# Kernel optimization log

Hardware: AMD Instinct MI355X
Metric: run time of the kernel (lower is better)

The kernel has to match this reference:

```python
import jax, jax.numpy as jnp
import numpy as np

B, N, E_PER = 2048, 64, 512            # graphs, nodes/graph, edges/graph
D_NODE, D_EMB = 16, 64                 # env.node_state_dim, node_embedding_size
D_USER, D_UEMB = 32, 64                # env.user_state_dim, user_embedding_size
HID = 512
TOTAL_N, TOTAL_E = B * N, B * E_PER


def setup_inputs() -> dict:
    key = jax.random.key(0)
    ks = jax.random.split(key, 16)
    off = (jnp.arange(B, dtype=jnp.int32) * N)[:, None]
    src = jax.random.randint(ks[0], (B, E_PER), 0, N, dtype=jnp.int32) + off
    dst = jax.random.randint(ks[1], (B, E_PER), 0, N, dtype=jnp.int32) + off
    edge_index = jnp.stack([src.reshape(-1), dst.reshape(-1)])  # [2, TOTAL_E]
    s = lambda k, shape, sc=0.05: jax.random.normal(k, shape, jnp.float32) * sc
    return {
        "x": jax.random.normal(ks[2], (TOTAL_N, D_NODE), jnp.float32),
        "edge_attr": jax.random.normal(ks[3], (TOTAL_E, 2), jnp.float32),
        "user_s": jax.random.normal(ks[4], (B, D_USER), jnp.float32),
        "W_msg": s(ks[5], (D_NODE, D_EMB)), "b_msg": jnp.zeros((D_EMB,), jnp.float32),
        "W_edge": s(ks[6], (2, D_EMB)),     "b_edge": jnp.zeros((D_EMB,), jnp.float32),
        "W_self": s(ks[7], (D_NODE, D_EMB)),"b_self": jnp.zeros((D_EMB,), jnp.float32),
        "W1": s(ks[8], (D_USER, D_UEMB)),   "b1": jnp.zeros((D_UEMB,), jnp.float32),
        "W2": s(ks[9], (N * D_EMB + D_UEMB, HID)), "b2": jnp.zeros((HID,), jnp.float32),
        "W3": s(ks[10], (HID, HID // 2)),   "b3": jnp.zeros((HID // 2,), jnp.float32),
        "W4": s(ks[11], (HID // 2, N), 0.01), "b4": jnp.zeros((N,), jnp.float32),
        "edge_index": edge_index,
    }


def reference(x, edge_attr, user_s, W_msg, b_msg, W_edge, b_edge, W_self, b_self,
              W1, b1, W2, b2, W3, b3, W4, b4, edge_index):
    src, dst = edge_index[0], edge_index[1]
    # GeneralConv (PyG): msg = lin_msg(x_j) + lin_edge(e); sum-aggregate at dst; + lin_self(x_i)
    msg = x[src] @ W_msg + b_msg + edge_attr @ W_edge + b_edge          # [TOTAL_E, D_EMB]
    agg = jax.ops.segment_sum(msg, dst, num_segments=TOTAL_N)          # [TOTAL_N, D_EMB]
    node = jax.nn.relu(agg + x @ W_self + b_self)
    # F.dropout(p=0.5, training=True) -- deterministic mask for the reference
    keep = jax.random.bernoulli(jax.random.key(42), 0.5, node.shape)
    node = jnp.where(keep, node * 2.0, 0.0)
    user = jax.nn.relu(user_s @ W1 + b1)                               # [B, D_UEMB]
    states = jnp.concatenate([node.reshape(B, N * D_EMB), user], axis=1)
    h = jax.nn.relu(states @ W2 + b2)
    h = jax.nn.relu(h @ W3 + b3)
    logits = h @ W4 + b4                                               # [B, N]
    # torch: unsqueeze(dim=0) then softmax(dim=1) => softmax across the BATCH axis
    return jax.nn.softmax(logits, axis=0)[None]                        # [1, B, N]
```

## Files before the change

kernel.cpp:

```cpp
#include <hip/hip_runtime.h>
#include <stdint.h>

#define B_GRAPHS 2048
#define CHUNK 256
#define E_PER 512
#define D_USER 32
#define HID 512
#define GK 4160
#define STATES_DIM 4160
#define WS_FALLBACK 6356992
#define WS_FAST 56197120

typedef unsigned short u16;
typedef unsigned int u32;
typedef __attribute__((ext_vector_type(8))) short short8;
typedef __attribute__((ext_vector_type(4))) float f32x4;

__device__ __forceinline__ float bf2f(u16 b) {
    union { uint32_t u; float f; } c; c.u = ((uint32_t)b) << 16; return c.f;
}
__device__ __forceinline__ u16 f2bf(float f) {
    union { float f; uint32_t u; } c; c.f = f;
    uint32_t u = c.u;
    return (u16)((u + 0x7FFFu + ((u >> 16) & 1u)) >> 16);
}
__device__ __forceinline__ void unpack2(uint32_t w, float& lo, float& hi) {
    union { uint32_t u; float f; } a, b;
    a.u = w << 16; b.u = w & 0xFFFF0000u;
    lo = a.f; hi = b.f;
}

__device__ __forceinline__ uint32_t rotl32(uint32_t v, int r) {
    return (v << r) | (v >> (32 - r));
}
__device__ __forceinline__ void threefry_0_42(uint32_t x0, uint32_t x1,
                                              uint32_t& o0, uint32_t& o1) {
    const uint32_t ks0 = 0u, ks1 = 42u, ks2 = 0x1BD11BDAu ^ 42u;
    x0 += ks0; x1 += ks1;
#define TFR(r) { x0 += x1; x1 = rotl32(x1, (r)); x1 ^= x0; }
    TFR(13) TFR(15) TFR(26) TFR(6)
    x0 += ks1; x1 += ks2 + 1u;
    TFR(17) TFR(29) TFR(16) TFR(24)
    x0 += ks2; x1 += ks0 + 2u;
    TFR(13) TFR(15) TFR(26) TFR(6)
    x0 += ks0; x1 += ks1 + 3u;
    TFR(17) TFR(29) TFR(16) TFR(24)
    x0 += ks1; x1 += ks2 + 4u;
    TFR(13) TFR(15) TFR(26) TFR(6)
    x0 += ks2; x1 += ks0 + 5u;
#undef TFR
    o0 = x0; o1 = x1;
}
__device__ __forceinline__ bool keep_bit(uint32_t j) {
    uint32_t o0, o1;
    threefry_0_42(0u, j, o0, o1);
    return (((o0 ^ o1) >> 31) == 0u);
}

__global__ __launch_bounds__(256) void fill_kernel(float* __restrict__ out, float v, int n) {
    int i = blockIdx.x * 256 + threadIdx.x;
    if (i < n) out[i] = v;
}

__device__ __forceinline__ void trans32(float (*sT)[33],
                                        const float* __restrict__ W,
                                        u16* __restrict__ WT,
                                        int K, int N, int k0, int n0, int tid) {
    const int tr = tid >> 5, tc = tid & 31;
    #pragma unroll
    for (int i = 0; i < 32; i += 8)
        sT[tr + i][tc] = W[(size_t)(k0 + tr + i) * N + n0 + tc];
    __syncthreads();
    #pragma unroll
    for (int i = 0; i < 32; i += 8)
        WT[(size_t)(n0 + tr + i) * K + k0 + tc] = f2bf(sT[tc][tr + i]);
}

#define SM_SCNT  0
#define SM_SXT   8192
#define SM_SA2   10496
#define SM_WCAT  15616
#define SM_ESUM  20736
#define SM_DEG   21248
#define SM_SIZE  21504

__global__ __launch_bounds__(256) void node_prep(
    const float* __restrict__ x, const float* __restrict__ edge_attr,
    const float* __restrict__ user_s,
    const float* __restrict__ W_msg, const float* __restrict__ W_self,
    const float* __restrict__ b_msg, const float* __restrict__ W_edge,
    const float* __restrict__ b_edge, const float* __restrict__ b_self,
    const float* __restrict__ W1, const float* __restrict__ b1,
    const int* __restrict__ src, const int* __restrict__ dst,
    const float* __restrict__ W2, u16* __restrict__ W2T,
    const float* __restrict__ W3, u16* __restrict__ W3T,
    const float* __restrict__ W4, u16* __restrict__ W4T,
    u16* __restrict__ states)
{
    __shared__ __align__(16) char smem[SM_SIZE];
    const int tid = threadIdx.x;

    if (blockIdx.x >= B_GRAPHS) {
        float (*sT)[33] = (float(*)[33])smem;
        int b = blockIdx.x - B_GRAPHS;
        if (b < 2080) {
            trans32(sT, W2, W2T, 4160, 512, (b % 130) * 32, (b / 130) * 32, tid);
            return;
        }
        b -= 2080;
        if (b < 128) {
            trans32(sT, W3, W3T, 512, 256, (b % 16) * 32, (b / 16) * 32, tid);
            return;
        }
        b -= 128;
        trans32(sT, W4, W4T, 256, 64, (b % 8) * 32, (b / 8) * 32, tid);
        return;
    }

    u32 (*scnt)[32]  = (u32(*)[32])(smem + SM_SCNT);
    u16 (*sxT)[72]   = (u16(*)[72])(smem + SM_SXT);
    u16 (*sA2)[40]   = (u16(*)[40])(smem + SM_SA2);
    u16* sWcat       = (u16*)(smem + SM_WCAT);
    float (*sesum)[64] = (float(*)[64])(smem + SM_ESUM);
    float* sdeg      = (float*)(smem + SM_DEG);

    const int g = blockIdx.x;
    const int w = tid >> 6, lane = tid & 63;
    const int lm = lane & 15, q = lane >> 4;

    const float* xg = x + (size_t)g * 1024;
    const float4 xv = *(const float4*)&xg[tid * 4];
    const int ge0 = g * E_PER + tid, ge1 = ge0 + 256;
    const int s0 = src[ge0] - g * 64, d0 = dst[ge0] - g * 64;
    const int s1 = src[ge1] - g * 64, d1 = dst[ge1] - g * 64;
    const float2* ea2 = (const float2*)edge_attr;
    const float2 a0 = ea2[ge0], a1 = ea2[ge1];
    float bs[4], bm[4], we0[4], we1[4];
    #pragma unroll
    for (int nt = 0; nt < 4; ++nt) {
        int e = nt * 16 + lm;
        bs[nt]  = b_self[e];
        bm[nt]  = b_msg[e] + b_edge[e];
        we0[nt] = W_edge[e];
        we1[nt] = W_edge[64 + e];
    }
    {
        uint4 z = make_uint4(0, 0, 0, 0);
        u32* c0 = &scnt[0][0] + tid * 8;
        *(uint4*)(c0) = z; *(uint4*)(c0 + 4) = z;
    }
    if (tid < 128) ((float*)sesum)[tid] = 0.f;
    {
        #pragma unroll
        for (int i = 0; i < 8; ++i) {
            int idx = tid + 256 * i;
            int e = idx >> 5, k = idx & 31;
            float v = (k < 16) ? W_msg[k * 64 + e] : W_self[(k - 16) * 64 + e];
            sWcat[e * 40 + k] = f2bf(v);
        }
    }
    {
        const int n = tid >> 2, kb = (tid & 3) * 4;
        u16 x0 = f2bf(xv.x), x1 = f2bf(xv.y), x2 = f2bf(xv.z), x3 = f2bf(xv.w);
        sxT[kb + 0][n] = x0; sxT[kb + 1][n] = x1;
        sxT[kb + 2][n] = x2; sxT[kb + 3][n] = x3;
        *(ushort4*)&sA2[n][16 + kb] = make_ushort4(x0, x1, x2, x3);
    }
    __syncthreads();

    atomicAdd(&scnt[d0][(s0 >> 1) ^ ((d0 & 7) << 2)], 1u << ((s0 & 1) * 16));
    atomicAdd(&scnt[d1][(s1 >> 1) ^ ((d1 & 7) << 2)], 1u << ((s1 & 1) * 16));
    atomicAdd(&sesum[0][d0], a0.x);
    atomicAdd(&sesum[1][d0], a0.y);
    atomicAdd(&sesum[0][d1], a1.x);
    atomicAdd(&sesum[1][d1], a1.y);
    __syncthreads();

    {
        const int d = tid >> 2, sq = tid & 3;
        uint4 c0 = *(const uint4*)&scnt[d][sq * 8];
        uint4 c1 = *(const uint4*)&scnt[d][sq * 8 + 4];
        u32 cw[8] = {c0.x, c0.y, c0.z, c0.w, c1.x, c1.y, c1.z, c1.w};
        u32 pk[8];
        float degp = 0.f;
        #pragma unroll
        for (int j = 0; j < 8; ++j) {
            u32 lo = cw[j] & 0xFFFFu, hi = cw[j] >> 16;
            degp += (float)(lo + hi);
            pk[j] = (u32)f2bf((float)lo) | ((u32)f2bf((float)hi) << 16);
        }
        *(uint4*)&scnt[d][sq * 8]     = make_uint4(pk[0], pk[1], pk[2], pk[3]);
        *(uint4*)&scnt[d][sq * 8 + 4] = make_uint4(pk[4], pk[5], pk[6], pk[7]);
        degp += __shfl_xor(degp, 1, 64);
        degp += __shfl_xor(degp, 2, 64);
        if (sq == 0) sdeg[d] = degp;
    }

    f32x4 accS;
    #pragma unroll
    for (int r = 0; r < 4; ++r) accS[r] = 0.f;
    {
        const char* crow = (const char*)&scnt[16 * w + lm][0];
        const int sw = (lm & 7) << 4;
        #pragma unroll
        for (int kh = 0; kh < 2; ++kh) {
            short8 a = *(const short8*)(crow + (((kh * 64) + q * 16) ^ sw));
            short8 b = *(const short8*)&sxT[lm][kh * 32 + q * 8];
            accS = __builtin_amdgcn_mfma_f32_16x16x32_bf16(a, b, accS, 0, 0, 0);
        }
    }
    #pragma unroll
    for (int r = 0; r < 4; ++r)
        sA2[16 * w + q * 4 + r][lm] = f2bf(accS[r]);

    f32x4 acc2[4];
    #pragma unroll
    for (int nt = 0; nt < 4; ++nt)
        #pragma unroll
        for (int r = 0; r < 4; ++r) acc2[nt][r] = 0.f;
    short8 a2 = *(const short8*)&sA2[16 * w + lm][q * 8];
    #pragma unroll
    for (int nt = 0; nt < 4; ++nt) {
        short8 b2 = *(const short8*)&sWcat[(nt * 16 + lm) * 40 + q * 8];
        acc2[nt] = __builtin_amdgcn_mfma_f32_16x16x32_bf16(a2, b2, acc2[nt], 0, 0, 0);
    }

    u16* out = states + (size_t)g * STATES_DIM;
    #pragma unroll
    for (int r = 0; r < 4; ++r) {
        int n = 16 * w + q * 4 + r;
        float dg = sdeg[n], e0 = sesum[0][n], e1 = sesum[1][n];
        uint32_t jbase = (uint32_t)g * 4096u + (uint32_t)(n * 64 + lm);
        #pragma unroll
        for (int nt = 0; nt < 4; ++nt) {
            float v = acc2[nt][r] + bs[nt] + dg * bm[nt]
                    + e0 * we0[nt] + e1 * we1[nt];
            v = v > 0.f ? v : 0.f;
            v = keep_bit(jbase + (uint32_t)(nt * 16)) ? v * 2.0f : 0.0f;
            out[n * 64 + nt * 16 + lm] = f2bf(v);
        }
    }
    if (tid < 64) {
        float v = b1[tid];
        const float* us = user_s + (size_t)g * D_USER;
        #pragma unroll
        for (int k = 0; k < D_USER; ++k) v += us[k] * W1[k * 64 + tid];
        out[4096 + tid] = f2bf(v > 0.f ? v : 0.f);
    }
}

__global__ __launch_bounds__(256) void node_fb(
    int g0,
    const float* __restrict__ x, const float* __restrict__ edge_attr,
    const float* __restrict__ user_s,
    const float* __restrict__ W_msg, const float* __restrict__ b_msg,
    const float* __restrict__ W_edge, const float* __restrict__ b_edge,
    const float* __restrict__ W_self, const float* __restrict__ b_self,
    const float* __restrict__ W1, const float* __restrict__ b1,
    const int* __restrict__ src, const int* __restrict__ dst,
    float* __restrict__ states)
{
    const int g = g0 + blockIdx.x;
    const int tid = threadIdx.x;

    __shared__ float sx[64][16];
    __shared__ float sxsum[64][16];
    __shared__ float sesum[64][2];
    __shared__ float sdeg[64];
    __shared__ float sWmsg[16][64];
    __shared__ float sWself[16][64];
    __shared__ float sWedge[2][64];
    __shared__ float sbias[64];
    __shared__ float sbself[64];

    const float* xg = x + (size_t)g * 1024;
    for (int i = tid; i < 1024; i += 256) {
        sx[i >> 4][i & 15] = xg[i];
        ((float*)sxsum)[i] = 0.f;
        ((float*)sWmsg)[i] = W_msg[i];
        ((float*)sWself)[i] = W_self[i];
    }
    if (tid < 128) ((float*)sWedge)[tid] = W_edge[tid];
    if (tid < 64) {
        sbias[tid] = b_msg[tid] + b_edge[tid];
        sbself[tid] = b_self[tid];
        sdeg[tid] = 0.f;
        sesum[tid][0] = 0.f; sesum[tid][1] = 0.f;
    }
    __syncthreads();

    const float2* ea2 = (const float2*)edge_attr;
    for (int e = tid; e < E_PER; e += 256) {
        int ge = g * E_PER + e;
        int s = src[ge] - g * 64;
        int d = dst[ge] - g * 64;
        float2 a = ea2[ge];
        atomicAdd(&sdeg[d], 1.0f);
        atomicAdd(&sesum[d][0], a.x);
        atomicAdd(&sesum[d][1], a.y);
        #pragma unroll
        for (int k = 0; k < 16; ++k) atomicAdd(&sxsum[d][k], sx[s][k]);
    }
    __syncthreads();

    float* out = states + (size_t)blockIdx.x * STATES_DIM;
    #pragma unroll
    for (int i = 0; i < 16; ++i) {
        int idx = tid + 256 * i;
        int n = idx >> 6, e = idx & 63;
        float v = sbself[e] + sdeg[n] * sbias[e]
                + sesum[n][0] * sWedge[0][e] + sesum[n][1] * sWedge[1][e];
        #pragma unroll
        for (int k = 0; k < 16; ++k)
            v += sxsum[n][k] * sWmsg[k][e] + sx[n][k] * sWself[k][e];
        v = v > 0.f ? v : 0.f;
        v = keep_bit((uint32_t)g * 4096u + (uint32_t)idx) ? v * 2.0f : 0.0f;
        out[idx] = v;
    }
    if (tid < 64) {
        float v = b1[tid];
        const float* us = user_s + (size_t)g * D_USER;
        #pragma unroll
        for (int k = 0; k < D_USER; ++k) v += us[k] * W1[k * 64 + tid];
        out[4096 + tid] = v > 0.f ? v : 0.f;
    }
}

__global__ __launch_bounds__(256) void gemm64(
    const u16* __restrict__ A, const u16* __restrict__ BT,
    float* __restrict__ Cpart, int K, int Ksplit, int N, int ntiles,
    int pstride)
{
    const int cpx = gridDim.x >> 3;
    const int bid = blockIdx.x;
    const int wg  = (bid & 7) * cpx + (bid >> 3);
    const int nt  = wg % ntiles, mt = wg / ntiles;
    const int m0 = mt * 64, n0 = nt * 64;
    const int kb = blockIdx.y * Ksplit;

    __shared__ u16 sA[64][72];
    __shared__ u16 sB[64][72];

    const int tid = threadIdx.x;
    const int wave = tid >> 6, lane = tid & 63;
    const int wm = (wave & 1) * 32, wn = (wave >> 1) * 32;
    const int lm = lane & 15, q = lane >> 4;

    f32x4 acc00, acc01, acc10, acc11;
    #pragma unroll
    for (int r = 0; r < 4; ++r) {
        acc00[r] = 0.f; acc01[r] = 0.f; acc10[r] = 0.f; acc11[r] = 0.f;
    }

    const int arow = tid >> 2, aseg = (tid & 3) * 16;
    const u16* pa = &A [(size_t)(m0 + arow) * K + kb + aseg];
    const u16* pb = &BT[(size_t)(n0 + arow) * K + kb + aseg];
    uint4 ra0 = *(const uint4*)pa, ra1 = *(const uint4*)(pa + 8);
    uint4 rb0 = *(const uint4*)pb, rb1 = *(const uint4*)(pb + 8);

    for (int k0 = 0; k0 < Ksplit; k0 += 64) {
        __syncthreads();
        *(uint4*)&sA[arow][aseg]     = ra0;
        *(uint4*)&sA[arow][aseg + 8] = ra1;
        *(uint4*)&sB[arow][aseg]     = rb0;
        *(uint4*)&sB[arow][aseg + 8] = rb1;
        __syncthreads();
        if (k0 + 64 < Ksplit) {
            pa += 64; pb += 64;
            ra0 = *(const uint4*)pa; ra1 = *(const uint4*)(pa + 8);
            rb0 = *(const uint4*)pb; rb1 = *(const uint4*)(pb + 8);
        }
        #pragma unroll
        for (int kh = 0; kh < 2; ++kh) {
            short8 a0 = *(const short8*)&sA[wm + lm]     [kh * 32 + q * 8];
            short8 a1 = *(const short8*)&sA[wm + 16 + lm][kh * 32 + q * 8];
            short8 b0 = *(const short8*)&sB[wn + lm]     [kh * 32 + q * 8];
            short8 b1 = *(const short8*)&sB[wn + 16 + lm][kh * 32 + q * 8];
            acc00 = __builtin_amdgcn_mfma_f32_16x16x32_bf16(a0, b0, acc00, 0, 0, 0);
            acc01 = __builtin_amdgcn_mfma_f32_16x16x32_bf16(a0, b1, acc01, 0, 0, 0);
            acc10 = __builtin_amdgcn_mfma_f32_16x16x32_bf16(a1, b0, acc10, 0, 0, 0);
            acc11 = __builtin_amdgcn_mfma_f32_16x16x32_bf16(a1, b1, acc11, 0, 0, 0);
        }
    }

    float* Cp = Cpart + (size_t)blockIdx.y * pstride;
    #pragma unroll
    for (int r = 0; r < 4; ++r) {
        int m = m0 + wm + q * 4 + r;
        Cp[(size_t)m * N + n0 + wn + lm]              = acc00[r];
        Cp[(size_t)m * N + n0 + wn + 16 + lm]         = acc01[r];
        Cp[(size_t)(m + 16) * N + n0 + wn + lm]       = acc10[r];
        Cp[(size_t)(m + 16) * N + n0 + wn + 16 + lm]  = acc11[r];
    }
}

__global__ __launch_bounds__(256) void bias_relu_sum(
    const float* __restrict__ parts, int pstride, int nsplit,
    const float* __restrict__ bias, u16* __restrict__ out,
    int Nmask, int total4)
{
    int i = blockIdx.x * 256 + threadIdx.x;
    if (i >= total4) return;
    const int base = i * 4;
    float4 v = *(const float4*)&bias[base & Nmask];
    for (int s = 0; s < nsplit; ++s) {
        float4 p = *(const float4*)&parts[(size_t)s * pstride + base];
        v.x += p.x; v.y += p.y; v.z += p.z; v.w += p.w;
    }
    ushort4 o;
    o.x = f2bf(v.x > 0.f ? v.x : 0.f);
    o.y = f2bf(v.y > 0.f ? v.y : 0.f);
    o.z = f2bf(v.z > 0.f ? v.z : 0.f);
    o.w = f2bf(v.w > 0.f ? v.w : 0.f);
    *(ushort4*)&out[base] = o;
}

template<typename AT, typename CT, bool RELU>
__global__ __launch_bounds__(256) void gemm_any(
    const AT* __restrict__ A, const float* __restrict__ B,
    const float* __restrict__ bias, CT* __restrict__ C,
    int M, int N, int K)
{
    __shared__ float sA[32][72];
    __shared__ float sB[32][64];

    const int tid = threadIdx.x;
    const int tx = tid & 15;
    const int ty = tid >> 4;
    const int m0 = blockIdx.x * 64, n0 = blockIdx.y * 64;

    float acc[4][4] = {};

    for (int k0 = 0; k0 < K; k0 += 32) {
        if constexpr (sizeof(AT) == 4) {
            int r = tid >> 3;
            int c = (tid & 7) * 4;
            #pragma unroll
            for (int rr = 0; rr < 64; rr += 32) {
                float4 v = *(const float4*)&((const float*)A)[(size_t)(m0 + r + rr) * K + k0 + c];
                sA[c + 0][r + rr] = v.x; sA[c + 1][r + rr] = v.y;
                sA[c + 2][r + rr] = v.z; sA[c + 3][r + rr] = v.w;
            }
        } else {
            int m = tid >> 2;
            int c = (tid & 3) * 8;
            uint4 v = *(const uint4*)&((const u16*)A)[(size_t)(m0 + m) * K + k0 + c];
            unpack2(v.x, sA[c + 0][m], sA[c + 1][m]);
            unpack2(v.y, sA[c + 2][m], sA[c + 3][m]);
            unpack2(v.z, sA[c + 4][m], sA[c + 5][m]);
            unpack2(v.w, sA[c + 6][m], sA[c + 7][m]);
        }
        {
            int r = tid >> 3;
            int nc = (tid & 7) * 8;
            float4 v0 = *(const float4*)&B[(size_t)(k0 + r) * N + n0 + nc];
            float4 v1 = *(const float4*)&B[(size_t)(k0 + r) * N + n0 + nc + 4];
            sB[r][nc + 0] = v0.x; sB[r][nc + 1] = v0.y;
            sB[r][nc + 2] = v0.z; sB[r][nc + 3] = v0.w;
            sB[r][nc + 4] = v1.x; sB[r][nc + 5] = v1.y;
            sB[r][nc + 6] = v1.z; sB[r][nc + 7] = v1.w;
        }
        __syncthreads();
        #pragma unroll
        for (int kk = 0; kk < 32; ++kk) {
            float4 av = *(const float4*)&sA[kk][ty * 4];
            float4 bv = *(const float4*)&sB[kk][tx * 4];
            float a_[4] = {av.x, av.y, av.z, av.w};
            float b_[4] = {bv.x, bv.y, bv.z, bv.w};
            #pragma unroll
            for (int i = 0; i < 4; ++i)
                #pragma unroll
                for (int j = 0; j < 4; ++j)
                    acc[i][j] += a_[i] * b_[j];
        }
        __syncthreads();
    }

    #pragma unroll
    for (int i = 0; i < 4; ++i) {
        int m = m0 + ty * 4 + i;
        #pragma unroll
        for (int j = 0; j < 4; ++j) {
            int n = n0 + tx * 4 + j;
            float v = acc[i][j] + bias[n];
            if (RELU) v = v > 0.f ? v : 0.f;
            if constexpr (sizeof(CT) == 2) C[(size_t)m * N + n] = (CT)f2bf(v);
            else                           C[(size_t)m * N + n] = (CT)v;
        }
    }
}

__global__ __launch_bounds__(256) void softmax4(
    const float* __restrict__ parts, const float* __restrict__ b4,
    float* __restrict__ out)
{
    const int n = blockIdx.x;
    const int tid = threadIdx.x;
    __shared__ float sred[4];
    const int wid = tid >> 6, lane = tid & 63;
    const float bn = b4[n];

    float v[8];
    #pragma unroll
    for (int i = 0; i < 8; ++i) {
        int row = (tid + 256 * i) * 64 + n;
        float t = bn + parts[row] + parts[131072 + row]
                + parts[262144 + row] + parts[393216 + row];
        v[i] = (t > -1e30f && t < 1e30f) ? t : 0.0f;
    }

    float mx = -3.4e38f;
    #pragma unroll
    for (int i = 0; i < 8; ++i) mx = fmaxf(mx, v[i]);
    #pragma unroll
    for (int off = 32; off > 0; off >>= 1) mx = fmaxf(mx, __shfl_down(mx, off, 64));
    if (lane == 0) sred[wid] = mx;
    __syncthreads();
    if (tid == 0) sred[0] = fmaxf(fmaxf(sred[0], sred[1]), fmaxf(sred[2], sred[3]));
    __syncthreads();
    mx = sred[0];
    __syncthreads();

    float sum = 0.f;
    #pragma unroll
    for (int i = 0; i < 8; ++i) { v[i] = expf(v[i] - mx); sum += v[i]; }
    #pragma unroll
    for (int off = 32; off > 0; off >>= 1) sum += __shfl_down(sum, off, 64);
    if (lane == 0) sred[wid] = sum;
    __syncthreads();
    if (tid == 0) sred[0] = sred[0] + sred[1] + sred[2] + sred[3];
    __syncthreads();
    float inv = 1.0f / sred[0];
    #pragma unroll
    for (int i = 0; i < 8; ++i) out[(tid + 256 * i) * 64 + n] = v[i] * inv;
}

__global__ __launch_bounds__(256) void softmax_kernel(
    const float* __restrict__ logits, float* __restrict__ out)
{
    const int n = blockIdx.x;
    const int tid = threadIdx.x;
    __shared__ float sred[4];
    const int wid = tid >> 6, lane = tid & 63;

    float v[8];
    #pragma unroll
    for (int i = 0; i < 8; ++i) {
        float t = logits[(tid + 256 * i) * 64 + n];
        v[i] = (t > -1e30f && t < 1e30f) ? t : 0.0f;
    }

    float mx = -3.4e38f;
    #pragma unroll
    for (int i = 0; i < 8; ++i) mx = fmaxf(mx, v[i]);
    #pragma unroll
    for (int off = 32; off > 0; off >>= 1) mx = fmaxf(mx, __shfl_down(mx, off, 64));
    if (lane == 0) sred[wid] = mx;
    __syncthreads();
    if (tid == 0) sred[0] = fmaxf(fmaxf(sred[0], sred[1]), fmaxf(sred[2], sred[3]));
    __syncthreads();
    mx = sred[0];
    __syncthreads();

    float sum = 0.f;
    #pragma unroll
    for (int i = 0; i < 8; ++i) { v[i] = expf(v[i] - mx); sum += v[i]; }
    #pragma unroll
    for (int off = 32; off > 0; off >>= 1) sum += __shfl_down(sum, off, 64);
    if (lane == 0) sred[wid] = sum;
    __syncthreads();
    if (tid == 0) sred[0] = sred[0] + sred[1] + sred[2] + sred[3];
    __syncthreads();
    float inv = 1.0f / sred[0];
    #pragma unroll
    for (int i = 0; i < 8; ++i) out[(tid + 256 * i) * 64 + n] = v[i] * inv;
}

extern "C" void kernel_launch(void* const* d_in, const int* in_sizes, int n_in,
                              void* d_out, int out_size, void* d_ws, size_t ws_size,
                              hipStream_t stream) {
    if (ws_size < (size_t)WS_FALLBACK || n_in < 18) {
        fill_kernel<<<(out_size + 255) / 256, 256, 0, stream>>>((float*)d_out, 0.25f, out_size);
        return;
    }
    {
        const int expect[18] = {2097152, 2097152, 65536, 1024, 64, 128, 64,
                                1024, 64, 2048, 64, 2129920, 512, 131072, 256,
                                16384, 64, 2097152};
        bool ok = true;
        for (int i = 0; i < 18; ++i) ok = ok && (in_sizes[i] == expect[i]);
        if (!ok || out_size != 131072) {
            fill_kernel<<<(out_size + 255) / 256, 256, 0, stream>>>((float*)d_out, 0.125f, out_size);
            return;
        }
    }

    const float* x         = (const float*)d_in[0];
    const float* edge_attr = (const float*)d_in[1];
    const float* user_s    = (const float*)d_in[2];
    const float* W_msg     = (const float*)d_in[3];
    const float* b_msg     = (const float*)d_in[4];
    const float* W_edge    = (const float*)d_in[5];
    const float* b_edge    = (const float*)d_in[6];
    const float* W_self    = (const float*)d_in[7];
    const float* b_self    = (const float*)d_in[8];
    const float* W1        = (const float*)d_in[9];
    const float* b1        = (const float*)d_in[10];
    const float* W2        = (const float*)d_in[11];
    const float* b2        = (const float*)d_in[12];
    const float* W3        = (const float*)d_in[13];
    const float* b3        = (const float*)d_in[14];
    const float* W4        = (const float*)d_in[15];
    const float* b4        = (const float*)d_in[16];
    const int* edge_index  = (const int*)d_in[17];
    const int* src = edge_index;
    const int* dst = edge_index + B_GRAPHS * E_PER;

    float* logits = (float*)d_out;
    char* ws = (char*)d_ws;

    if (ws_size >= (size_t)WS_FAST) {
        u16*   states = (u16*)ws;
        u16*   W2T    = (u16*)(ws + 17039360);
        float* h2part = (float*)(ws + 21299200);
        u16*   h2     = (u16*)(ws + 42270720);
        u16*   W3T    = (u16*)(ws + 44367872);
        float* h3part = (float*)(ws + 44630016);
        u16*   h3     = (u16*)(ws + 53018624);
        u16*   W4T    = (u16*)(ws + 54067200);
        float* lpart  = (float*)(ws + 54099968);

        node_prep<<<B_GRAPHS + 2224, 256, 0, stream>>>(
            x, edge_attr, user_s, W_msg, W_self, b_msg, W_edge, b_edge,
            b_self, W1, b1, src, dst, W2, W2T, W3, W3T, W4, W4T, states);
        gemm64<<<dim3(256, 5), 256, 0, stream>>>(states, W2T, h2part,
                                                 GK, 832, 512, 8, 1048576);
        bias_relu_sum<<<1024, 256, 0, stream>>>(h2part, 1048576, 5, b2, h2,
                                                511, 262144);
        gemm64<<<dim3(128, 4), 256, 0, stream>>>(h2, W3T, h3part,
                                                 512, 128, 256, 4, 524288);
        bias_relu_sum<<<512, 256, 0, stream>>>(h3part, 524288, 4, b3, h3,
                                               255, 131072);
        gemm64<<<dim3(32, 4), 256, 0, stream>>>(h3, W4T, lpart,
                                                256, 64, 64, 1, 131072);
        softmax4<<<64, 256, 0, stream>>>(lpart, b4, logits);
    } else {
        float* states = (float*)ws;
        float* h3     = (float*)ws;
        u16*   h2     = (u16*)(ws + 4259840);

        for (int c = 0; c < B_GRAPHS / CHUNK; ++c) {
            node_fb<<<CHUNK, 256, 0, stream>>>(
                c * CHUNK, x, edge_attr, user_s, W_msg, b_msg, W_edge, b_edge,
                W_self, b_self, W1, b1, src, dst, states);
            gemm_any<float, u16, true><<<dim3(CHUNK / 64, HID / 64), 256, 0, stream>>>(
                states, W2, b2, h2 + (size_t)c * CHUNK * HID, CHUNK, HID, STATES_DIM);
        }
        gemm_any<u16,   float, true ><<<dim3(32, 4), 256, 0, stream>>>(
            h2, W3, b3, h3, B_GRAPHS, HID / 2, HID);
        gemm_any<float, float, false><<<dim3(32, 1), 256, 0, stream>>>(
            h3, W4, b4, logits, B_GRAPHS, 64, HID / 2);
        softmax_kernel<<<64, 256, 0, stream>>>(logits, logits);
    }
}
```

Measured before the change: 174.7 us.

## Use direct global-to-LDS loads with swizzle in GEMM, fuse final layer into softmax

Result: slower. 192.1 us (+9.9%).

```diff
diff --git a/kernel.cpp b/kernel.cpp
--- a/kernel.cpp
+++ b/kernel.cpp
@@ -9,7 +9,7 @@
 #define GK 4160
 #define STATES_DIM 4160
 #define WS_FALLBACK 6356992
-#define WS_FAST 56197120
+#define WS_FAST 54067200
 
 typedef unsigned short u16;
 typedef unsigned int u32;
@@ -28,6 +28,12 @@
     union { uint32_t u; float f; } a, b;
     a.u = w << 16; b.u = w & 0xFFFF0000u;
     lo = a.f; hi = b.f;
+}
+
+__device__ __forceinline__ void gload16(const u16* g, u16* l) {
+    __builtin_amdgcn_global_load_lds(
+        (const __attribute__((address_space(1))) void*)g,
+        (__attribute__((address_space(3))) void*)l, 16, 0, 0);
 }
 
 __device__ __forceinline__ uint32_t rotl32(uint32_t v, int r) {
@@ -94,7 +100,6 @@
     const int* __restrict__ src, const int* __restrict__ dst,
     const float* __restrict__ W2, u16* __restrict__ W2T,
     const float* __restrict__ W3, u16* __restrict__ W3T,
-    const float* __restrict__ W4, u16* __restrict__ W4T,
     u16* __restrict__ states)
 {
     __shared__ __align__(16) char smem[SM_SIZE];
@@ -105,15 +110,10 @@
         int b = blockIdx.x - B_GRAPHS;
         if (b < 2080) {
             trans32(sT, W2, W2T, 4160, 512, (b % 130) * 32, (b / 130) * 32, tid);
-            return;
-        }
-        b -= 2080;
-        if (b < 128) {
+        } else {
+            b -= 2080;
             trans32(sT, W3, W3T, 512, 256, (b % 16) * 32, (b / 16) * 32, tid);
-            return;
-        }
-        b -= 128;
-        trans32(sT, W4, W4T, 256, 64, (b % 8) * 32, (b / 8) * 32, tid);
+        }
         return;
     }
 
@@ -150,6 +150,15 @@
         *(uint4*)(c0) = z; *(uint4*)(c0 + 4) = z;
     }
     if (tid < 128) ((float*)sesum)[tid] = 0.f;
+    u32 kmask = 0;
+    #pragma unroll
+    for (int r = 0; r < 4; ++r) {
+        const uint32_t jb = (uint32_t)g * 4096u
+                          + (uint32_t)((16 * w + q * 4 + r) * 64 + lm);
+        #pragma unroll
+        for (int nt = 0; nt < 4; ++nt)
+            if (keep_bit(jb + (uint32_t)(nt * 16))) kmask |= 1u << (r * 4 + nt);
+    }
     {
         #pragma unroll
         for (int i = 0; i < 8; ++i) {
@@ -230,13 +239,12 @@
     for (int r = 0; r < 4; ++r) {
         int n = 16 * w + q * 4 + r;
         float dg = sdeg[n], e0 = sesum[0][n], e1 = sesum[1][n];
-        uint32_t jbase = (uint32_t)g * 4096u + (uint32_t)(n * 64 + lm);
         #pragma unroll
         for (int nt = 0; nt < 4; ++nt) {
             float v = acc2[nt][r] + bs[nt] + dg * bm[nt]
                     + e0 * we0[nt] + e1 * we1[nt];
             v = v > 0.f ? v : 0.f;
-            v = keep_bit(jbase + (uint32_t)(nt * 16)) ? v * 2.0f : 0.0f;
+            v = ((kmask >> (r * 4 + nt)) & 1u) ? v * 2.0f : 0.0f;
             out[n * 64 + nt * 16 + lm] = f2bf(v);
         }
     }
@@ -338,8 +346,8 @@
     const int m0 = mt * 64, n0 = nt * 64;
     const int kb = blockIdx.y * Ksplit;
 
-    __shared__ u16 sA[64][72];
-    __shared__ u16 sB[64][72];
+    __shared__ u16 sA[64][64];
+    __shared__ u16 sB[64][64];
 
     const int tid = threadIdx.x;
     const int wave = tid >> 6, lane = tid & 63;
@@ -352,35 +360,41 @@
         acc00[r] = 0.f; acc01[r] = 0.f; acc10[r] = 0.f; acc11[r] = 0.f;
     }
 
-    const int arow = tid >> 2, aseg = (tid & 3) * 16;
-    const u16* pa = &A [(size_t)(m0 + arow) * K + kb + aseg];
-    const u16* pb = &BT[(size_t)(n0 + arow) * K + kb + aseg];
-    uint4 ra0 = *(const uint4*)pa, ra1 = *(const uint4*)(pa + 8);
-    uint4 rb0 = *(const uint4*)pb, rb1 = *(const uint4*)(pb + 8);
+    const int srow  = wave * 8 + (lane >> 3);
+    const int selem = 8 * ((lane & 7) ^ (lane >> 3));
+    const u16* pa0 = &A [(size_t)(m0 + srow) * K + kb + selem];
+    const u16* pa1 = &A [(size_t)(m0 + 32 + srow) * K + kb + selem];
+    const u16* pb0 = &BT[(size_t)(n0 + srow) * K + kb + selem];
+    const u16* pb1 = &BT[(size_t)(n0 + 32 + srow) * K + kb + selem];
+    u16* lA0 = (u16*)((char*)&sA[0][0] + wave * 1024);
+    u16* lA1 = (u16*)((char*)&sA[0][0] + 4096 + wave * 1024);
+    u16* lB0 = (u16*)((char*)&sB[0][0] + wave * 1024);
+    u16* lB1 = (u16*)((char*)&sB[0][0] + 4096 + wave * 1024);
+
+    const int sw = (lm & 7) << 4;
+    const char* cA  = (const char*)sA + (wm + lm) * 128;
+    const char* cA2 = cA + 16 * 128;
+    const char* cB  = (const char*)sB + (wn + lm) * 128;
+    const char* cB2 = cB + 16 * 128;
 
     for (int k0 = 0; k0 < Ksplit; k0 += 64) {
+        gload16(pa0, lA0); gload16(pa1, lA1);
+        gload16(pb0, lB0); gload16(pb1, lB1);
+        pa0 += 64; pa1 += 64; pb0 += 64; pb1 += 64;
         __syncthreads();
-        *(uint4*)&sA[arow][aseg]     = ra0;
-        *(uint4*)&sA[arow][aseg + 8] = ra1;
-        *(uint4*)&sB[arow][aseg]     = rb0;
-        *(uint4*)&sB[arow][aseg + 8] = rb1;
-        __syncthreads();
-        if (k0 + 64 < Ksplit) {
-            pa += 64; pb += 64;
-            ra0 = *(const uint4*)pa; ra1 = *(const uint4*)(pa + 8);
-            rb0 = *(const uint4*)pb; rb1 = *(const uint4*)(pb + 8);
-        }
         #pragma unroll
         for (int kh = 0; kh < 2; ++kh) {
-            short8 a0 = *(const short8*)&sA[wm + lm]     [kh * 32 + q * 8];
-            short8 a1 = *(const short8*)&sA[wm + 16 + lm][kh * 32 + q * 8];
-            short8 b0 = *(const short8*)&sB[wn + lm]     [kh * 32 + q * 8];
-            short8 b1 = *(const short8*)&sB[wn + 16 + lm][kh * 32 + q * 8];
+            const int off = (kh * 64 + q * 16) ^ sw;
+            short8 a0 = *(const short8*)(cA  + off);
+            short8 a1 = *(const short8*)(cA2 + off);
+            short8 b0 = *(const short8*)(cB  + off);
+            short8 b1 = *(const short8*)(cB2 + off);
             acc00 = __builtin_amdgcn_mfma_f32_16x16x32_bf16(a0, b0, acc00, 0, 0, 0);
             acc01 = __builtin_amdgcn_mfma_f32_16x16x32_bf16(a0, b1, acc01, 0, 0, 0);
             acc10 = __builtin_amdgcn_mfma_f32_16x16x32_bf16(a1, b0, acc10, 0, 0, 0);
             acc11 = __builtin_amdgcn_mfma_f32_16x16x32_bf16(a1, b1, acc11, 0, 0, 0);
         }
+        __syncthreads();
     }
 
     float* Cp = Cpart + (size_t)blockIdx.y * pstride;
@@ -490,49 +504,69 @@
     }
 }
 
-__global__ __launch_bounds__(256) void softmax4(
-    const float* __restrict__ parts, const float* __restrict__ b4,
-    float* __restrict__ out)
+__global__ __launch_bounds__(512) void gemv_softmax(
+    const u16* __restrict__ h3, const float* __restrict__ W4,
+    const float* __restrict__ b4, float* __restrict__ out)
 {
     const int n = blockIdx.x;
     const int tid = threadIdx.x;
-    __shared__ float sred[4];
+    __shared__ float sw4[256];
+    __shared__ float sred[8];
     const int wid = tid >> 6, lane = tid & 63;
+
+    if (tid < 256) sw4[tid] = W4[tid * 64 + n];
+    __syncthreads();
     const float bn = b4[n];
 
-    float v[8];
-    #pragma unroll
-    for (int i = 0; i < 8; ++i) {
-        int row = (tid + 256 * i) * 64 + n;
-        float t = bn + parts[row] + parts[131072 + row]
-                + parts[262144 + row] + parts[393216 + row];
-        v[i] = (t > -1e30f && t < 1e30f) ? t : 0.0f;
-    }
-
-    float mx = -3.4e38f;
-    #pragma unroll
-    for (int i = 0; i < 8; ++i) mx = fmaxf(mx, v[i]);
+    float v[4];
+    #pragma unroll
+    for (int i = 0; i < 4; ++i) {
+        const u16* row = h3 + (size_t)(tid + 512 * i) * 256;
+        float acc = bn;
+        #pragma unroll 4
+        for (int k = 0; k < 256; k += 8) {
+            uint4 hv = *(const uint4*)&row[k];
+            float lo, hi;
+            unpack2(hv.x, lo, hi); acc += lo * sw4[k]     + hi * sw4[k + 1];
+            unpack2(hv.y, lo, hi); acc += lo * sw4[k + 2] + hi * sw4[k + 3];
+            unpack2(hv.z, lo, hi); acc += lo * sw4[k + 4] + hi * sw4[k + 5];
+            unpack2(hv.w, lo, hi); acc += lo * sw4[k + 6] + hi * sw4[k + 7];
+        }
+        v[i] = (acc > -1e30f && acc < 1e30f) ? acc : 0.0f;
+    }
+
+    float mx = fmaxf(fmaxf(v[0], v[1]), fmaxf(v[2], v[3]));
     #pragma unroll
     for (int off = 32; off > 0; off >>= 1) mx = fmaxf(mx, __shfl_down(mx, off, 64));
     if (lane == 0) sred[wid] = mx;
     __syncthreads();
-    if (tid == 0) sred[0] = fmaxf(fmaxf(sred[0], sred[1]), fmaxf(sred[2], sred[3]));
+    if (tid == 0) {
+        float m = sred[0];
+        #pragma unroll
+        for (int j = 1; j < 8; ++j) m = fmaxf(m, sred[j]);
+        sred[0] = m;
+    }
     __syncthreads();
     mx = sred[0];
     __syncthreads();
 
     float sum = 0.f;
     #pragma unroll
-    for (int i = 0; i < 8; ++i) { v[i] = expf(v[i] - mx); sum += v[i]; }
+    for (int i = 0; i < 4; ++i) { v[i] = expf(v[i] - mx); sum += v[i]; }
     #pragma unroll
     for (int off = 32; off > 0; off >>= 1) sum += __shfl_down(sum, off, 64);
     if (lane == 0) sred[wid] = sum;
     __syncthreads();
-    if (tid == 0) sred[0] = sred[0] + sred[1] + sred[2] + sred[3];
+    if (tid == 0) {
+        float s = 0.f;
+        #pragma unroll
+        for (int j = 0; j < 8; ++j) s += sred[j];
+        sred[0] = s;
+    }
     __syncthreads();
     float inv = 1.0f / sred[0];
     #pragma unroll
-    for (int i = 0; i < 8; ++i) out[(tid + 256 * i) * 64 + n] = v[i] * inv;
+    for (int i = 0; i < 4; ++i) out[(tid + 512 * i) * 64 + n] = v[i] * inv;
 }
 
 __global__ __launch_bounds__(256) void softmax_kernel(
@@ -627,12 +661,10 @@
         u16*   W3T    = (u16*)(ws + 44367872);
         float* h3part = (float*)(ws + 44630016);
         u16*   h3     = (u16*)(ws + 53018624);
-        u16*   W4T    = (u16*)(ws + 54067200);
-        float* lpart  = (float*)(ws + 54099968);
-
-        node_prep<<<B_GRAPHS + 2224, 256, 0, stream>>>(
+
+        node_prep<<<B_GRAPHS + 2208, 256, 0, stream>>>(
             x, edge_attr, user_s, W_msg, W_self, b_msg, W_edge, b_edge,
-            b_self, W1, b1, src, dst, W2, W2T, W3, W3T, W4, W4T, states);
+            b_self, W1, b1, src, dst, W2, W2T, W3, W3T, states);
         gemm64<<<dim3(256, 5), 256, 0, stream>>>(states, W2T, h2part,
                                                  GK, 832, 512, 8, 1048576);
         bias_relu_sum<<<1024, 256, 0, stream>>>(h2part, 1048576, 5, b2, h2,
@@ -641,9 +673,7 @@
                                                  512, 128, 256, 4, 524288);
         bias_relu_sum<<<512, 256, 0, stream>>>(h3part, 524288, 4, b3, h3,
                                                255, 131072);
-        gemm64<<<dim3(32, 4), 256, 0, stream>>>(h3, W4T, lpart,
-                                                256, 64, 64, 1, 131072);
-        softmax4<<<64, 256, 0, stream>>>(lpart, b4, logits);
+        gemv_softmax<<<64, 512, 0, stream>>>(h3, W4, b4, logits);
     } else {
         float* states = (float*)ws;
         float* h3     = (float*)ws;
```

## Use async global-to-LDS double buffering in gemm64 and precompute dropout mask via ballot

Applied to the files above, without the earlier changes.

After: 183.4 us. 5.0% more time.

```diff
diff --git a/kernel.cpp b/kernel.cpp
--- a/kernel.cpp
+++ b/kernel.cpp
@@ -28,6 +28,12 @@
     union { uint32_t u; float f; } a, b;
     a.u = w << 16; b.u = w & 0xFFFF0000u;
     lo = a.f; hi = b.f;
+}
+
+__device__ __forceinline__ void gload16(const u16* g, u16* l) {
+    __builtin_amdgcn_global_load_lds(
+        (const __attribute__((address_space(1))) void*)g,
+        (__attribute__((address_space(3))) void*)l, 16, 0, 0);
 }
 
 __device__ __forceinline__ uint32_t rotl32(uint32_t v, int r) {
@@ -82,7 +88,8 @@
 #define SM_WCAT  15616
 #define SM_ESUM  20736
 #define SM_DEG   21248
-#define SM_SIZE  21504
+#define SM_MASK  21504
+#define SM_SIZE  22016
 
 __global__ __launch_bounds__(256) void node_prep(
     const float* __restrict__ x, const float* __restrict__ edge_attr,
@@ -123,6 +130,7 @@
     u16* sWcat       = (u16*)(smem + SM_WCAT);
     float (*sesum)[64] = (float(*)[64])(smem + SM_ESUM);
     float* sdeg      = (float*)(smem + SM_DEG);
+    unsigned long long* smask = (unsigned long long*)(smem + SM_MASK);
 
     const int g = blockIdx.x;
     const int w = tid >> 6, lane = tid & 63;
@@ -166,6 +174,12 @@
         sxT[kb + 2][n] = x2; sxT[kb + 3][n] = x3;
         *(ushort4*)&sA2[n][16 + kb] = make_ushort4(x0, x1, x2, x3);
     }
+    #pragma unroll 4
+    for (int i = 0; i < 16; ++i) {
+        unsigned long long b =
+            __ballot(keep_bit((uint32_t)g * 4096u + (uint32_t)(i * 256 + tid)));
+        if (lane == 0) smask[i * 4 + w] = b;
+    }
     __syncthreads();
 
     atomicAdd(&scnt[d0][(s0 >> 1) ^ ((d0 & 7) << 2)], 1u << ((s0 & 1) * 16));
@@ -230,14 +244,15 @@
     for (int r = 0; r < 4; ++r) {
         int n = 16 * w + q * 4 + r;
         float dg = sdeg[n], e0 = sesum[0][n], e1 = sesum[1][n];
-        uint32_t jbase = (uint32_t)g * 4096u + (uint32_t)(n * 64 + lm);
+        unsigned long long m = smask[n];
         #pragma unroll
         for (int nt = 0; nt < 4; ++nt) {
             float v = acc2[nt][r] + bs[nt] + dg * bm[nt]
                     + e0 * we0[nt] + e1 * we1[nt];
             v = v > 0.f ? v : 0.f;
-            v = keep_bit(jbase + (uint32_t)(nt * 16)) ? v * 2.0f : 0.0f;
-            out[n * 64 + nt * 16 + lm] = f2bf(v);
+            int e = nt * 16 + lm;
+            v = ((m >> e) & 1ull) ? v * 2.0f : 0.0f;
+            out[n * 64 + e] = f2bf(v);
         }
     }
     if (tid < 64) {
@@ -338,8 +353,7 @@
     const int m0 = mt * 64, n0 = nt * 64;
     const int kb = blockIdx.y * Ksplit;
 
-    __shared__ u16 sA[64][72];
-    __shared__ u16 sB[64][72];
+    __shared__ __align__(16) char smem[32768];
 
     const int tid = threadIdx.x;
     const int wave = tid >> 6, lane = tid & 63;
@@ -352,35 +366,52 @@
         acc00[r] = 0.f; acc01[r] = 0.f; acc10[r] = 0.f; acc11[r] = 0.f;
     }
 
-    const int arow = tid >> 2, aseg = (tid & 3) * 16;
-    const u16* pa = &A [(size_t)(m0 + arow) * K + kb + aseg];
-    const u16* pb = &BT[(size_t)(n0 + arow) * K + kb + aseg];
-    uint4 ra0 = *(const uint4*)pa, ra1 = *(const uint4*)(pa + 8);
-    uint4 rb0 = *(const uint4*)pb, rb1 = *(const uint4*)(pb + 8);
-
-    for (int k0 = 0; k0 < Ksplit; k0 += 64) {
-        __syncthreads();
-        *(uint4*)&sA[arow][aseg]     = ra0;
-        *(uint4*)&sA[arow][aseg + 8] = ra1;
-        *(uint4*)&sB[arow][aseg]     = rb0;
-        *(uint4*)&sB[arow][aseg + 8] = rb1;
-        __syncthreads();
-        if (k0 + 64 < Ksplit) {
-            pa += 64; pb += 64;
-            ra0 = *(const uint4*)pa; ra1 = *(const uint4*)(pa + 8);
-            rb0 = *(const uint4*)pb; rb1 = *(const uint4*)(pb + 8);
-        }
+    const int srow  = wave * 8 + (lane >> 3);
+    const int selem = 8 * ((lane & 7) ^ (lane >> 3));
+    const u16* pa0 = &A [(size_t)(m0 + srow) * K + kb + selem];
+    const u16* pa1 = &A [(size_t)(m0 + 32 + srow) * K + kb + selem];
+    const u16* pb0 = &BT[(size_t)(n0 + srow) * K + kb + selem];
+    const u16* pb1 = &BT[(size_t)(n0 + 32 + srow) * K + kb + selem];
+    const int woff = wave * 1024;
+
+    const int sw = (lm & 7) << 4;
+    const int nsteps = Ksplit >> 6;
+
+    gload16(pa0, (u16*)(smem + woff));
+    gload16(pa1, (u16*)(smem + 4096 + woff));
+    gload16(pb0, (u16*)(smem + 16384 + woff));
+    gload16(pb1, (u16*)(smem + 16384 + 4096 + woff));
+    pa0 += 64; pa1 += 64; pb0 += 64; pb1 += 64;
+    __syncthreads();
+
+    int cur = 0;
+    for (int t = 0; t < nsteps; ++t) {
+        if (t + 1 < nsteps) {
+            const int nb = (cur ^ 1) * 8192;
+            gload16(pa0, (u16*)(smem + nb + woff));
+            gload16(pa1, (u16*)(smem + nb + 4096 + woff));
+            gload16(pb0, (u16*)(smem + 16384 + nb + woff));
+            gload16(pb1, (u16*)(smem + 16384 + nb + 4096 + woff));
+            pa0 += 64; pa1 += 64; pb0 += 64; pb1 += 64;
+        }
+        const char* cA  = smem + cur * 8192 + (wm + lm) * 128;
+        const char* cA2 = cA + 16 * 128;
+        const char* cB  = smem + 16384 + cur * 8192 + (wn + lm) * 128;
+        const char* cB2 = cB + 16 * 128;
         #pragma unroll
         for (int kh = 0; kh < 2; ++kh) {
-            short8 a0 = *(const short8*)&sA[wm + lm]     [kh * 32 + q * 8];
-            short8 a1 = *(const short8*)&sA[wm + 16 + lm][kh * 32 + q * 8];
-            short8 b0 = *(const short8*)&sB[wn + lm]     [kh * 32 + q * 8];
-            short8 b1 = *(const short8*)&sB[wn + 16 + lm][kh * 32 + q * 8];
+            const int off = (kh * 64 + q * 16) ^ sw;
+            short8 a0 = *(const short8*)(cA  + off);
+            short8 a1 = *(const short8*)(cA2 + off);
+            short8 b0 = *(const short8*)(cB  + off);
+            short8 b1 = *(const short8*)(cB2 + off);
             acc00 = __builtin_amdgcn_mfma_f32_16x16x32_bf16(a0, b0, acc00, 0, 0, 0);
             acc01 = __builtin_amdgcn_mfma_f32_16x16x32_bf16(a0, b1, acc01, 0, 0, 0);
             acc10 = __builtin_amdgcn_mfma_f32_16x16x32_bf16(a1, b0, acc10, 0, 0, 0);
             acc11 = __builtin_amdgcn_mfma_f32_16x16x32_bf16(a1, b1, acc11, 0, 0, 0);
         }
+        __syncthreads();
+        cur ^= 1;
     }
 
     float* Cp = Cpart + (size_t)blockIdx.y * pstride;
```
